# Kernel optimization log

Measured on AMD Instinct MI355X. Metric: run time of the kernel, lower is better.

The kernel has to match this reference:

```python
import jax, jax.numpy as jnp
import numpy as np

K = 2  # num_experts_per_token


def setup_inputs() -> dict:
    key = jax.random.key(0)
    ks = jax.random.split(key, 5)
    B, T, D, E, H = 2, 2048, 768, 8, 1536
    x = jax.random.normal(ks[0], (B, T, D), dtype=jnp.float32)
    gate_w = jax.random.normal(ks[1], (E, D), dtype=jnp.float32) * (1.0 / np.sqrt(D))
    gate_bank = jax.random.normal(ks[2], (E, D, H), dtype=jnp.float32) * (1.0 / np.sqrt(D))
    up_bank = jax.random.normal(ks[3], (E, D, H), dtype=jnp.float32) * (1.0 / np.sqrt(D))
    down_bank = jax.random.normal(ks[4], (E, H, D), dtype=jnp.float32) * (1.0 / np.sqrt(H))
    return {"x": x, "gate_w": gate_w, "gate_bank": gate_bank,
            "up_bank": up_bank, "down_bank": down_bank}


def reference(x, gate_w, gate_bank, up_bank, down_bank):
    # x: [B,T,D]; gate_w: [E,D]; banks: [E,D,H]/[E,D,H]/[E,H,D]
    # Eval mode: no gate noise (module only adds noise when training).
    logits = jnp.einsum('btd,ed->bte', x, gate_w)                  # [B,T,E]
    probs = jax.nn.softmax(logits, axis=-1)
    selected_probs, selected_idx = jax.lax.top_k(probs, K)          # [B,T,K]
    selected_probs = selected_probs / (
        jnp.sum(selected_probs, axis=-1, keepdims=True) + 1e-8)

    a = jnp.einsum('btd,edh->bteh', x, gate_bank)                   # [B,T,E,H]
    u = jnp.einsum('btd,edh->bteh', x, up_bank)
    h = jax.nn.silu(a) * u
    y_all = jnp.einsum('bteh,ehd->bted', h, down_bank)              # [B,T,E,D]

    # Gather the top-k experts' outputs and combine with normalized weights.
    y_sel = jnp.take_along_axis(y_all, selected_idx[..., None], axis=2)  # [B,T,K,D]
    y = jnp.sum(y_sel * selected_probs[..., None], axis=2)          # [B,T,D]
    return y
```

## Files before the change

kernel.cpp:

```cpp
#include <hip/hip_runtime.h>
#include <hip/hip_bf16.h>

#define NTOK 4096
#define DDIM 768
#define EEXP 8
#define HDIM 1536
#define MBLK 128
#define MAXMB 72
#define CAP  (MAXMB * MBLK)
#define NENT (NTOK * 2)
#define RTHREADS 1024
#define EPT (NENT / RTHREADS)
#define NTTILE 6912

typedef float f32x4 __attribute__((ext_vector_type(4)));
typedef __bf16 bf16x8 __attribute__((ext_vector_type(8)));
typedef __bf16 bf16x4 __attribute__((ext_vector_type(4)));

static const size_t XB_OFF   = 0;
static const size_t GT_OFF   = 6291456;
static const size_t UT_OFF   = GT_OFF + 18874368;
static const size_t YB_OFF   = GT_OFF;
static const size_t DT_OFF   = UT_OFF + 18874368;
static const size_t HB_OFF   = DT_OFF + 18874368;
static const size_t TKI_OFF  = HB_OFF + 28311552;
static const size_t TKW_OFF  = TKI_OFF + NENT*4;
static const size_t PT_OFF   = TKW_OFF + NENT*4;
static const size_t SL_OFF   = PT_OFF + CAP*4;
static const size_t CTRL_OFF = SL_OFF + NENT*4;
static const size_t WS_NEEDED = CTRL_OFF + 1024;

#define GLOAD16(g, l) __builtin_amdgcn_global_load_lds( \
    (const __attribute__((address_space(1))) void*)(g),  \
    (__attribute__((address_space(3))) void*)(l), 16, 0, 0)

#define MFMA_BF16 __builtin_amdgcn_mfma_f32_16x16x32_bf16


__global__ __launch_bounds__(256) void gating_kernel(
    const float* __restrict__ x, const float* __restrict__ gw,
    int* __restrict__ topk_idx, float* __restrict__ topk_w,
    __bf16* __restrict__ xb)
{
    int lane = threadIdx.x & 63;
    int t = blockIdx.x * 4 + (threadIdx.x >> 6);
    const float* xr = x + (size_t)t * DDIM;
    __bf16* xbr = xb + (size_t)t * DDIM;
    float acc[EEXP];
#pragma unroll
    for (int e = 0; e < EEXP; e++) acc[e] = 0.0f;
#pragma unroll
    for (int i = 0; i < DDIM / 64; i++) {
        int d = lane + i * 64;
        float xv = xr[d];
        xbr[d] = (__bf16)xv;
#pragma unroll
        for (int e = 0; e < EEXP; e++) acc[e] += xv * gw[e * DDIM + d];
    }
#pragma unroll
    for (int e = 0; e < EEXP; e++) {
        for (int off = 32; off; off >>= 1) acc[e] += __shfl_xor(acc[e], off);
    }
    if (lane == 0) {
        float m = acc[0];
#pragma unroll
        for (int e = 1; e < EEXP; e++) m = fmaxf(m, acc[e]);
        float p[EEXP], sum = 0.0f;
#pragma unroll
        for (int e = 0; e < EEXP; e++) { p[e] = expf(acc[e] - m); sum += p[e]; }
        int i0 = 0; float b0 = acc[0];
#pragma unroll
        for (int e = 1; e < EEXP; e++) if (acc[e] > b0) { b0 = acc[e]; i0 = e; }
        int i1 = -1; float b1 = -3.4e38f;
#pragma unroll
        for (int e = 0; e < EEXP; e++) if (e != i0 && acc[e] > b1) { b1 = acc[e]; i1 = e; }
        float pr0 = p[i0] / sum, pr1 = p[i1] / sum;
        float den = pr0 + pr1 + 1e-8f;
        topk_idx[2*t]   = i0; topk_w[2*t]   = pr0 / den;
        topk_idx[2*t+1] = i1; topk_w[2*t+1] = pr1 / den;
    }
}

__global__ __launch_bounds__(RTHREADS) void mega_kernel(
    const float* __restrict__ gb, const float* __restrict__ ub,
    const float* __restrict__ db, __bf16* __restrict__ Gt,
    __bf16* __restrict__ Ut, __bf16* __restrict__ Dt,
    const int* __restrict__ topk_idx, int* __restrict__ ctrl,
    int* __restrict__ pair_token, int* __restrict__ slot_of)
{
    __shared__ float tile[64][65];
    __shared__ int wt[EEXP][16];
    __shared__ int wpre[EEXP][16];
    __shared__ int base[EEXP];

    int tid = threadIdx.x;

    if (blockIdx.x == 0) {
        int lane = tid & 63, wv = tid >> 6;
        for (int i = tid; i < CAP; i += RTHREADS) pair_token[i] = 0;

        int e_of[EPT];
        int c[EEXP];
#pragma unroll
        for (int e = 0; e < EEXP; e++) c[e] = 0;
#pragma unroll
        for (int j = 0; j < EPT; j++) {
            int e = topk_idx[tid * EPT + j];
            e_of[j] = e;
            c[e]++;
        }
        int pre[EEXP];
#pragma unroll
        for (int e = 0; e < EEXP; e++) {
            int v = c[e];
            for (int d = 1; d < 64; d <<= 1) {
                int u = __shfl_up(v, d);
                if (lane >= d) v += u;
            }
            pre[e] = v - c[e];
            if (lane == 63) wt[e][wv] = v;
        }
        __syncthreads();
        if (tid == 0) {
            int off = 0, gmb = 0;
            for (int e = 0; e < EEXP; e++) {
                int run = 0;
                for (int w = 0; w < 16; w++) { wpre[e][w] = run; run += wt[e][w]; }
                base[e] = off;
                int nmb = (run + MBLK - 1) >> 7;
                for (int i = 0; i < nmb; i++) ctrl[32 + gmb++] = e;
                off += nmb << 7;
            }
            ctrl[24] = gmb;
        }
        __syncthreads();
        int run[EEXP];
#pragma unroll
        for (int e = 0; e < EEXP; e++) run[e] = base[e] + wpre[e][wv] + pre[e];
#pragma unroll
        for (int j = 0; j < EPT; j++) {
            int ent = tid * EPT + j;
            int e = e_of[j];
            int slot = run[e]++;
            pair_token[slot] = ent >> 1;
            slot_of[ent] = slot;
        }
        return;
    }

    int bt = blockIdx.x - 1;
    int z = bt / 288, rem = bt - z * 288;
    int bank = z >> 3, e = z & 7;
    int R, C, r0, c0;
    const float* s;
    __bf16* d;
    if (bank < 2) {
        R = DDIM; C = HDIM;
        s = (bank == 0 ? gb : ub) + (size_t)e * DDIM * HDIM;
        d = (bank == 0 ? Gt : Ut) + (size_t)e * DDIM * HDIM;
        c0 = (rem % 24) * 64; r0 = (rem / 24) * 64;
    } else {
        R = HDIM; C = DDIM;
        s = db + (size_t)e * DDIM * HDIM;
        d = Dt + (size_t)e * DDIM * HDIM;
        r0 = (rem % 24) * 64; c0 = (rem / 24) * 64;
    }
    int tx = tid & 15, ty = tid >> 4;
    {
        f32x4 v = *reinterpret_cast<const f32x4*>(&s[(size_t)(r0 + ty) * C + c0 + tx * 4]);
        tile[ty][tx*4+0] = v[0]; tile[ty][tx*4+1] = v[1];
        tile[ty][tx*4+2] = v[2]; tile[ty][tx*4+3] = v[3];
    }
    __syncthreads();
    {
        bf16x4 o;
#pragma unroll
        for (int i = 0; i < 4; i++) o[i] = (__bf16)tile[tx*4+i][ty];
        *reinterpret_cast<bf16x4*>(&d[(size_t)(c0 + ty) * R + r0 + tx*4]) = o;
    }
}

__global__ __launch_bounds__(256, 2) void gateup_kernel(
    const __bf16* __restrict__ xb, const __bf16* __restrict__ Gt,
    const __bf16* __restrict__ Ut, const int* __restrict__ ctrl,
    const int* __restrict__ pair_token, __bf16* __restrict__ hbuf)
{
    int bid = blockIdx.x;
    int swz = (bid & 7) * (MAXMB * 12 / 8) + (bid >> 3);
    int mb = swz / 12, y = swz - mb * 12;
    if (mb >= ctrl[24]) return;
    int e = ctrl[32 + mb];
    int hbase = y * 128;
    const __bf16* G = Gt + (size_t)e * HDIM * DDIM;
    const __bf16* U = Ut + (size_t)e * HDIM * DDIM;

    __shared__ __bf16 lds[3 * 8192];

    int tid = threadIdx.x;
    int lane = tid & 63, w = tid >> 6;
    int wr = w >> 1, wc = w & 1;

    int lr = tid >> 3;
    int lc = ((tid & 7) ^ (lr & 7)) << 3;
    const __bf16* gA[4];
#pragma unroll
    for (int j = 0; j < 4; j++) {
        int tok = pair_token[mb * MBLK + j * 32 + lr];
        gA[j] = xb + (size_t)tok * DDIM + lc;
    }
    const __bf16* gG = G + (size_t)(hbase + lr) * DDIM + lc;
    const __bf16* gU = U + (size_t)(hbase + lr) * DDIM + lc;
    const size_t rstep = (size_t)32 * DDIM;

    f32x4 accg[4][4], accu[4][4];
#pragma unroll
    for (int m = 0; m < 4; m++)
#pragma unroll
        for (int n = 0; n < 4; n++) { accg[m][n] = (f32x4)0.0f; accu[m][n] = (f32x4)0.0f; }

#pragma unroll
    for (int kt = 0; kt < DDIM / 64; kt++) {
        const int kk = kt * 64;
#pragma unroll
        for (int j = 0; j < 4; j++)
            GLOAD16(gA[j] + kk, &lds[j * 2048 + tid * 8]);
#pragma unroll
        for (int j = 0; j < 4; j++)
            GLOAD16(gG + kk + j * rstep, &lds[8192 + j * 2048 + tid * 8]);
#pragma unroll
        for (int j = 0; j < 4; j++)
            GLOAD16(gU + kk + j * rstep, &lds[16384 + j * 2048 + tid * 8]);
        __syncthreads();

#pragma unroll
        for (int ks = 0; ks < 2; ks++) {
            int kb = ks * 32 + (lane >> 4) * 8;
            bf16x8 af[4], bg[4], bu[4];
#pragma unroll
            for (int m = 0; m < 4; m++) {
                int row = wr * 64 + m * 16 + (lane & 15);
                af[m] = *reinterpret_cast<const bf16x8*>(
                    &lds[row * 64 + (kb ^ ((row & 7) << 3))]);
            }
#pragma unroll
            for (int n = 0; n < 4; n++) {
                int col = wc * 64 + n * 16 + (lane & 15);
                int ba = col * 64 + (kb ^ ((col & 7) << 3));
                bg[n] = *reinterpret_cast<const bf16x8*>(&lds[8192 + ba]);
                bu[n] = *reinterpret_cast<const bf16x8*>(&lds[16384 + ba]);
            }
#pragma unroll
            for (int n = 0; n < 4; n++)
#pragma unroll
                for (int m = 0; m < 4; m++) {
                    accg[m][n] = MFMA_BF16(af[m], bg[n], accg[m][n], 0, 0, 0);
                    accu[m][n] = MFMA_BF16(af[m], bu[n], accu[m][n], 0, 0, 0);
                }
        }
        __syncthreads();
    }

    size_t slotbase = (size_t)mb * MBLK;
#pragma unroll
    for (int m = 0; m < 4; m++)
#pragma unroll
        for (int n = 0; n < 4; n++)
#pragma unroll
            for (int r = 0; r < 4; r++) {
                int row = wr * 64 + m * 16 + (lane >> 4) * 4 + r;
                int col = hbase + wc * 64 + n * 16 + (lane & 15);
                float a = accg[m][n][r], u = accu[m][n][r];
                float hv = (a / (1.0f + expf(-a))) * u;
                hbuf[(slotbase + row) * HDIM + col] = (__bf16)hv;
            }
}

__global__ __launch_bounds__(256, 3) void down_kernel(
    const __bf16* __restrict__ hbuf, const __bf16* __restrict__ Dt,
    const int* __restrict__ ctrl, float* __restrict__ ybuf)
{
    int bid = blockIdx.x;
    int swz = (bid & 7) * (MAXMB * 6 / 8) + (bid >> 3);
    int mb = swz / 6, y = swz - mb * 6;
    if (mb >= ctrl[24]) return;
    int e = ctrl[32 + mb];
    int dbase = y * 128;
    const __bf16* Dn = Dt + (size_t)e * DDIM * HDIM;

    __shared__ __bf16 lds[2 * 8192];

    int tid = threadIdx.x;
    int lane = tid & 63, w = tid >> 6;
    int wr = w >> 1, wc = w & 1;

    int lr = tid >> 3;
    int lc = ((tid & 7) ^ (lr & 7)) << 3;
    const __bf16* gA = hbuf + (size_t)(mb * MBLK + lr) * HDIM + lc;
    const __bf16* gB = Dn + (size_t)(dbase + lr) * HDIM + lc;
    const size_t rstep = (size_t)32 * HDIM;

    f32x4 acc[4][4];
#pragma unroll
    for (int m = 0; m < 4; m++)
#pragma unroll
        for (int n = 0; n < 4; n++) acc[m][n] = (f32x4)0.0f;

#pragma unroll
    for (int kt = 0; kt < HDIM / 64; kt++) {
        const int kk = kt * 64;
#pragma unroll
        for (int j = 0; j < 4; j++)
            GLOAD16(gA + kk + j * rstep, &lds[j * 2048 + tid * 8]);
#pragma unroll
        for (int j = 0; j < 4; j++)
            GLOAD16(gB + kk + j * rstep, &lds[8192 + j * 2048 + tid * 8]);
        __syncthreads();

#pragma unroll
        for (int ks = 0; ks < 2; ks++) {
            int kb = ks * 32 + (lane >> 4) * 8;
            bf16x8 af[4], bd[4];
#pragma unroll
            for (int m = 0; m < 4; m++) {
                int row = wr * 64 + m * 16 + (lane & 15);
                af[m] = *reinterpret_cast<const bf16x8*>(
                    &lds[row * 64 + (kb ^ ((row & 7) << 3))]);
            }
#pragma unroll
            for (int n = 0; n < 4; n++) {
                int col = wc * 64 + n * 16 + (lane & 15);
                bd[n] = *reinterpret_cast<const bf16x8*>(
                    &lds[8192 + col * 64 + (kb ^ ((col & 7) << 3))]);
            }
#pragma unroll
            for (int n = 0; n < 4; n++)
#pragma unroll
                for (int m = 0; m < 4; m++)
                    acc[m][n] = MFMA_BF16(af[m], bd[n], acc[m][n], 0, 0, 0);
        }
        __syncthreads();
    }

#pragma unroll
    for (int m = 0; m < 4; m++)
#pragma unroll
        for (int n = 0; n < 4; n++)
#pragma unroll
            for (int r = 0; r < 4; r++) {
                int row = wr * 64 + m * 16 + (lane >> 4) * 4 + r;
                int col = dbase + wc * 64 + n * 16 + (lane & 15);
                ybuf[(size_t)(mb * MBLK + row) * DDIM + col] = acc[m][n][r];
            }
}

__global__ __launch_bounds__(192) void combine_kernel(
    const float* __restrict__ ybuf, const int* __restrict__ slot_of,
    const float* __restrict__ topk_w, float* __restrict__ out)
{
    int t = blockIdx.x;
    int q = threadIdx.x;
    int s0 = slot_of[2*t], s1 = slot_of[2*t+1];
    float w0 = topk_w[2*t], w1 = topk_w[2*t+1];
    f32x4 y0 = reinterpret_cast<const f32x4*>(ybuf + (size_t)s0 * DDIM)[q];
    f32x4 y1 = reinterpret_cast<const f32x4*>(ybuf + (size_t)s1 * DDIM)[q];
    f32x4 o;
#pragma unroll
    for (int r = 0; r < 4; r++) o[r] = w0 * y0[r] + w1 * y1[r];
    reinterpret_cast<f32x4*>(out + (size_t)t * DDIM)[q] = o;
}

extern "C" void kernel_launch(void* const* d_in, const int* in_sizes, int n_in,
                              void* d_out, int out_size, void* d_ws, size_t ws_size,
                              hipStream_t stream)
{
    if (ws_size < WS_NEEDED) return;

    const float* x      = (const float*)d_in[0];
    const float* gate_w = (const float*)d_in[1];
    const float* gbank  = (const float*)d_in[2];
    const float* ubank  = (const float*)d_in[3];
    const float* dbank  = (const float*)d_in[4];
    float* out = (float*)d_out;

    char* ws = (char*)d_ws;
    __bf16* xb   = (__bf16*)(ws + XB_OFF);
    __bf16* Gt   = (__bf16*)(ws + GT_OFF);
    __bf16* Ut   = (__bf16*)(ws + UT_OFF);
    float*  ybuf = (float*)(ws + YB_OFF);
    __bf16* Dt   = (__bf16*)(ws + DT_OFF);
    __bf16* hbuf = (__bf16*)(ws + HB_OFF);
    int*    tki  = (int*)(ws + TKI_OFF);
    float*  tkw  = (float*)(ws + TKW_OFF);
    int*    pt   = (int*)(ws + PT_OFF);
    int*    slot = (int*)(ws + SL_OFF);
    int*    ctrl = (int*)(ws + CTRL_OFF);

    gating_kernel<<<NTOK / 4, 256, 0, stream>>>(x, gate_w, tki, tkw, xb);
    mega_kernel<<<NTTILE + 1, RTHREADS, 0, stream>>>(
        gbank, ubank, dbank, Gt, Ut, Dt, tki, ctrl, pt, slot);

    gateup_kernel<<<MAXMB * (HDIM / 128), 256, 0, stream>>>(xb, Gt, Ut, ctrl, pt, hbuf);
    down_kernel<<<MAXMB * (DDIM / 128), 256, 0, stream>>>(hbuf, Dt, ctrl, ybuf);
    combine_kernel<<<NTOK, 192, 0, stream>>>(ybuf, slot, tkw, out);
}
```

Baseline: 125.4 us.

## Switch GEMMs to 32x32x16 MFMA and fuse gating into weight-transpose prep kernel

Both grouped GEMM kernels now use the 32x32x16 bf16 MFMA with 2x2 fragments per wave instead of 4x4 fragments of 16x16x32, which halves the LDS fragment reads per k-step. The gating/top-k work is merged into the transpose kernel as extra blocks, and routing is split into a separate single-block kernel. The transpose blocks drop from 1024 to 256 threads, each handling four rows. Together this cuts LDS traffic and gives better occupancy in the prep phase, at the cost of one extra launch for routing.

```diff
diff --git a/kernel.cpp b/kernel.cpp
--- a/kernel.cpp
+++ b/kernel.cpp
@@ -11,9 +11,11 @@
 #define NENT (NTOK * 2)
 #define RTHREADS 1024
 #define EPT (NENT / RTHREADS)
+#define NGATE (NTOK / 4)
 #define NTTILE 6912
 
 typedef float f32x4 __attribute__((ext_vector_type(4)));
+typedef float f32x16 __attribute__((ext_vector_type(16)));
 typedef __bf16 bf16x8 __attribute__((ext_vector_type(8)));
 typedef __bf16 bf16x4 __attribute__((ext_vector_type(4)));
 
@@ -34,121 +36,62 @@
     (const __attribute__((address_space(1))) void*)(g),  \
     (__attribute__((address_space(3))) void*)(l), 16, 0, 0)
 
-#define MFMA_BF16 __builtin_amdgcn_mfma_f32_16x16x32_bf16
-
-
-__global__ __launch_bounds__(256) void gating_kernel(
+#define MFMA32 __builtin_amdgcn_mfma_f32_32x32x16_bf16
+
+
+__global__ __launch_bounds__(256) void prep_kernel(
     const float* __restrict__ x, const float* __restrict__ gw,
     int* __restrict__ topk_idx, float* __restrict__ topk_w,
-    __bf16* __restrict__ xb)
-{
-    int lane = threadIdx.x & 63;
-    int t = blockIdx.x * 4 + (threadIdx.x >> 6);
-    const float* xr = x + (size_t)t * DDIM;
-    __bf16* xbr = xb + (size_t)t * DDIM;
-    float acc[EEXP];
-#pragma unroll
-    for (int e = 0; e < EEXP; e++) acc[e] = 0.0f;
-#pragma unroll
-    for (int i = 0; i < DDIM / 64; i++) {
-        int d = lane + i * 64;
-        float xv = xr[d];
-        xbr[d] = (__bf16)xv;
-#pragma unroll
-        for (int e = 0; e < EEXP; e++) acc[e] += xv * gw[e * DDIM + d];
-    }
-#pragma unroll
-    for (int e = 0; e < EEXP; e++) {
-        for (int off = 32; off; off >>= 1) acc[e] += __shfl_xor(acc[e], off);
-    }
-    if (lane == 0) {
-        float m = acc[0];
-#pragma unroll
-        for (int e = 1; e < EEXP; e++) m = fmaxf(m, acc[e]);
-        float p[EEXP], sum = 0.0f;
-#pragma unroll
-        for (int e = 0; e < EEXP; e++) { p[e] = expf(acc[e] - m); sum += p[e]; }
-        int i0 = 0; float b0 = acc[0];
-#pragma unroll
-        for (int e = 1; e < EEXP; e++) if (acc[e] > b0) { b0 = acc[e]; i0 = e; }
-        int i1 = -1; float b1 = -3.4e38f;
-#pragma unroll
-        for (int e = 0; e < EEXP; e++) if (e != i0 && acc[e] > b1) { b1 = acc[e]; i1 = e; }
-        float pr0 = p[i0] / sum, pr1 = p[i1] / sum;
-        float den = pr0 + pr1 + 1e-8f;
-        topk_idx[2*t]   = i0; topk_w[2*t]   = pr0 / den;
-        topk_idx[2*t+1] = i1; topk_w[2*t+1] = pr1 / den;
-    }
-}
-
-__global__ __launch_bounds__(RTHREADS) void mega_kernel(
+    __bf16* __restrict__ xb,
     const float* __restrict__ gb, const float* __restrict__ ub,
     const float* __restrict__ db, __bf16* __restrict__ Gt,
-    __bf16* __restrict__ Ut, __bf16* __restrict__ Dt,
-    const int* __restrict__ topk_idx, int* __restrict__ ctrl,
-    int* __restrict__ pair_token, int* __restrict__ slot_of)
+    __bf16* __restrict__ Ut, __bf16* __restrict__ Dt)
 {
     __shared__ float tile[64][65];
-    __shared__ int wt[EEXP][16];
-    __shared__ int wpre[EEXP][16];
-    __shared__ int base[EEXP];
-
     int tid = threadIdx.x;
 
-    if (blockIdx.x == 0) {
-        int lane = tid & 63, wv = tid >> 6;
-        for (int i = tid; i < CAP; i += RTHREADS) pair_token[i] = 0;
-
-        int e_of[EPT];
-        int c[EEXP];
-#pragma unroll
-        for (int e = 0; e < EEXP; e++) c[e] = 0;
-#pragma unroll
-        for (int j = 0; j < EPT; j++) {
-            int e = topk_idx[tid * EPT + j];
-            e_of[j] = e;
-            c[e]++;
-        }
-        int pre[EEXP];
+    if (blockIdx.x < NGATE) {
+        int lane = tid & 63;
+        int t = blockIdx.x * 4 + (tid >> 6);
+        const float* xr = x + (size_t)t * DDIM;
+        __bf16* xbr = xb + (size_t)t * DDIM;
+        float acc[EEXP];
+#pragma unroll
+        for (int e = 0; e < EEXP; e++) acc[e] = 0.0f;
+#pragma unroll
+        for (int i = 0; i < DDIM / 64; i++) {
+            int d = lane + i * 64;
+            float xv = xr[d];
+            xbr[d] = (__bf16)xv;
+#pragma unroll
+            for (int e = 0; e < EEXP; e++) acc[e] += xv * gw[e * DDIM + d];
+        }
 #pragma unroll
         for (int e = 0; e < EEXP; e++) {
-            int v = c[e];
-            for (int d = 1; d < 64; d <<= 1) {
-                int u = __shfl_up(v, d);
-                if (lane >= d) v += u;
-            }
-            pre[e] = v - c[e];
-            if (lane == 63) wt[e][wv] = v;
-        }
-        __syncthreads();
-        if (tid == 0) {
-            int off = 0, gmb = 0;
-            for (int e = 0; e < EEXP; e++) {
-                int run = 0;
-                for (int w = 0; w < 16; w++) { wpre[e][w] = run; run += wt[e][w]; }
-                base[e] = off;
-                int nmb = (run + MBLK - 1) >> 7;
-                for (int i = 0; i < nmb; i++) ctrl[32 + gmb++] = e;
-                off += nmb << 7;
-            }
-            ctrl[24] = gmb;
-        }
-        __syncthreads();
-        int run[EEXP];
-#pragma unroll
-        for (int e = 0; e < EEXP; e++) run[e] = base[e] + wpre[e][wv] + pre[e];
-#pragma unroll
-        for (int j = 0; j < EPT; j++) {
-            int ent = tid * EPT + j;
-            int e = e_of[j];
-            int slot = run[e]++;
-            pair_token[slot] = ent >> 1;
-            slot_of[ent] = slot;
+            for (int off = 32; off; off >>= 1) acc[e] += __shfl_xor(acc[e], off);
+        }
+        if (lane == 0) {
+            float m = acc[0];
+#pragma unroll
+            for (int e = 1; e < EEXP; e++) m = fmaxf(m, acc[e]);
+            float p[EEXP], sum = 0.0f;
+#pragma unroll
+            for (int e = 0; e < EEXP; e++) { p[e] = expf(acc[e] - m); sum += p[e]; }
+            int i0 = 0; float b0 = acc[0];
+#pragma unroll
+            for (int e = 1; e < EEXP; e++) if (acc[e] > b0) { b0 = acc[e]; i0 = e; }
+            int i1 = -1; float b1 = -3.4e38f;
+#pragma unroll
+            for (int e = 0; e < EEXP; e++) if (e != i0 && acc[e] > b1) { b1 = acc[e]; i1 = e; }
+            float pr0 = p[i0] / sum, pr1 = p[i1] / sum;
+            float den = pr0 + pr1 + 1e-8f;
+            topk_idx[2*t]   = i0; topk_w[2*t]   = pr0 / den;
+            topk_idx[2*t+1] = i1; topk_w[2*t+1] = pr1 / den;
         }
         return;
     }
 
-    int bt = blockIdx.x - 1;
+    int bt = blockIdx.x - NGATE;
     int z = bt / 288, rem = bt - z * 288;
     int bank = z >> 3, e = z & 7;
     int R, C, r0, c0;
@@ -166,17 +109,82 @@
         r0 = (rem % 24) * 64; c0 = (rem / 24) * 64;
     }
     int tx = tid & 15, ty = tid >> 4;
-    {
-        f32x4 v = *reinterpret_cast<const f32x4*>(&s[(size_t)(r0 + ty) * C + c0 + tx * 4]);
-        tile[ty][tx*4+0] = v[0]; tile[ty][tx*4+1] = v[1];
-        tile[ty][tx*4+2] = v[2]; tile[ty][tx*4+3] = v[3];
+#pragma unroll
+    for (int j = 0; j < 4; j++) {
+        int r = ty + j * 16;
+        f32x4 v = *reinterpret_cast<const f32x4*>(&s[(size_t)(r0 + r) * C + c0 + tx * 4]);
+        tile[r][tx*4+0] = v[0]; tile[r][tx*4+1] = v[1];
+        tile[r][tx*4+2] = v[2]; tile[r][tx*4+3] = v[3];
     }
     __syncthreads();
-    {
+#pragma unroll
+    for (int j = 0; j < 4; j++) {
+        int c = ty + j * 16;
         bf16x4 o;
 #pragma unroll
-        for (int i = 0; i < 4; i++) o[i] = (__bf16)tile[tx*4+i][ty];
-        *reinterpret_cast<bf16x4*>(&d[(size_t)(c0 + ty) * R + r0 + tx*4]) = o;
+        for (int i = 0; i < 4; i++) o[i] = (__bf16)tile[tx*4+i][c];
+        *reinterpret_cast<bf16x4*>(&d[(size_t)(c0 + c) * R + r0 + tx*4]) = o;
+    }
+}
+
+__global__ __launch_bounds__(RTHREADS) void route_kernel(
+    const int* __restrict__ topk_idx, int* __restrict__ ctrl,
+    int* __restrict__ pair_token, int* __restrict__ slot_of)
+{
+    __shared__ int wt[EEXP][16];
+    __shared__ int wpre[EEXP][16];
+    __shared__ int base[EEXP];
+
+    int tid = threadIdx.x;
+    int lane = tid & 63, wv = tid >> 6;
+
+    for (int i = tid; i < CAP; i += RTHREADS) pair_token[i] = 0;
+
+    int e_of[EPT];
+    int c[EEXP];
+#pragma unroll
+    for (int e = 0; e < EEXP; e++) c[e] = 0;
+#pragma unroll
+    for (int j = 0; j < EPT; j++) {
+        int e = topk_idx[tid * EPT + j];
+        e_of[j] = e;
+        c[e]++;
+    }
+    int pre[EEXP];
+#pragma unroll
+    for (int e = 0; e < EEXP; e++) {
+        int v = c[e];
+        for (int d = 1; d < 64; d <<= 1) {
+            int u = __shfl_up(v, d);
+            if (lane >= d) v += u;
+        }
+        pre[e] = v - c[e];
+        if (lane == 63) wt[e][wv] = v;
+    }
+    __syncthreads();
+    if (tid == 0) {
+        int off = 0, gmb = 0;
+        for (int e = 0; e < EEXP; e++) {
+            int run = 0;
+            for (int w = 0; w < 16; w++) { wpre[e][w] = run; run += wt[e][w]; }
+            base[e] = off;
+            int nmb = (run + MBLK - 1) >> 7;
+            for (int i = 0; i < nmb; i++) ctrl[32 + gmb++] = e;
+            off += nmb << 7;
+        }
+        ctrl[24] = gmb;
+    }
+    __syncthreads();
+    int run[EEXP];
+#pragma unroll
+    for (int e = 0; e < EEXP; e++) run[e] = base[e] + wpre[e][wv] + pre[e];
+#pragma unroll
+    for (int j = 0; j < EPT; j++) {
+        int ent = tid * EPT + j;
+        int e = e_of[j];
+        int slot = run[e]++;
+        pair_token[slot] = ent >> 1;
+        slot_of[ent] = slot;
     }
 }
 
@@ -212,11 +220,11 @@
     const __bf16* gU = U + (size_t)(hbase + lr) * DDIM + lc;
     const size_t rstep = (size_t)32 * DDIM;
 
-    f32x4 accg[4][4], accu[4][4];
-#pragma unroll
-    for (int m = 0; m < 4; m++)
-#pragma unroll
-        for (int n = 0; n < 4; n++) { accg[m][n] = (f32x4)0.0f; accu[m][n] = (f32x4)0.0f; }
+    f32x16 accg[2][2], accu[2][2];
+#pragma unroll
+    for (int m = 0; m < 2; m++)
+#pragma unroll
+        for (int n = 0; n < 2; n++) { accg[m][n] = (f32x16)0.0f; accu[m][n] = (f32x16)0.0f; }
 
 #pragma unroll
     for (int kt = 0; kt < DDIM / 64; kt++) {
@@ -233,42 +241,43 @@
         __syncthreads();
 
 #pragma unroll
-        for (int ks = 0; ks < 2; ks++) {
-            int kb = ks * 32 + (lane >> 4) * 8;
-            bf16x8 af[4], bg[4], bu[4];
-#pragma unroll
-            for (int m = 0; m < 4; m++) {
-                int row = wr * 64 + m * 16 + (lane & 15);
+        for (int s = 0; s < 4; s++) {
+            int kb = s * 16 + (lane >> 5) * 8;
+            bf16x8 af[2], bg[2], bu[2];
+#pragma unroll
+            for (int m = 0; m < 2; m++) {
+                int row = wr * 64 + m * 32 + (lane & 31);
                 af[m] = *reinterpret_cast<const bf16x8*>(
                     &lds[row * 64 + (kb ^ ((row & 7) << 3))]);
             }
 #pragma unroll
-            for (int n = 0; n < 4; n++) {
-                int col = wc * 64 + n * 16 + (lane & 15);
+            for (int n = 0; n < 2; n++) {
+                int col = wc * 64 + n * 32 + (lane & 31);
                 int ba = col * 64 + (kb ^ ((col & 7) << 3));
                 bg[n] = *reinterpret_cast<const bf16x8*>(&lds[8192 + ba]);
                 bu[n] = *reinterpret_cast<const bf16x8*>(&lds[16384 + ba]);
             }
 #pragma unroll
-            for (int n = 0; n < 4; n++)
-#pragma unroll
-                for (int m = 0; m < 4; m++) {
-                    accg[m][n] = MFMA_BF16(af[m], bg[n], accg[m][n], 0, 0, 0);
-                    accu[m][n] = MFMA_BF16(af[m], bu[n], accu[m][n], 0, 0, 0);
+            for (int n = 0; n < 2; n++)
+#pragma unroll
+                for (int m = 0; m < 2; m++) {
+                    accg[m][n] = MFMA32(af[m], bg[n], accg[m][n], 0, 0, 0);
+                    accu[m][n] = MFMA32(af[m], bu[n], accu[m][n], 0, 0, 0);
                 }
         }
         __syncthreads();
     }
 
     size_t slotbase = (size_t)mb * MBLK;
-#pragma unroll
-    for (int m = 0; m < 4; m++)
-#pragma unroll
-        for (int n = 0; n < 4; n++)
-#pragma unroll
-            for (int r = 0; r < 4; r++) {
-                int row = wr * 64 + m * 16 + (lane >> 4) * 4 + r;
-                int col = hbase + wc * 64 + n * 16 + (lane & 15);
+    int hi4 = (lane >> 5) * 4;
+#pragma unroll
+    for (int m = 0; m < 2; m++)
+#pragma unroll
+        for (int n = 0; n < 2; n++)
+#pragma unroll
+            for (int r = 0; r < 16; r++) {
+                int row = wr * 64 + m * 32 + (r & 3) + 8 * (r >> 2) + hi4;
+                int col = hbase + wc * 64 + n * 32 + (lane & 31);
                 float a = accg[m][n][r], u = accu[m][n][r];
                 float hv = (a / (1.0f + expf(-a))) * u;
                 hbuf[(slotbase + row) * HDIM + col] = (__bf16)hv;
@@ -299,11 +308,11 @@
     const __bf16* gB = Dn + (size_t)(dbase + lr) * HDIM + lc;
     const size_t rstep = (size_t)32 * HDIM;
 
-    f32x4 acc[4][4];
-#pragma unroll
-    for (int m = 0; m < 4; m++)
-#pragma unroll
-        for (int n = 0; n < 4; n++) acc[m][n] = (f32x4)0.0f;
+    f32x16 acc[2][2];
+#pragma unroll
+    for (int m = 0; m < 2; m++)
+#pragma unroll
+        for (int n = 0; n < 2; n++) acc[m][n] = (f32x16)0.0f;
 
 #pragma unroll
     for (int kt = 0; kt < HDIM / 64; kt++) {
@@ -317,38 +326,39 @@
         __syncthreads();
 
 #pragma unroll
-        for (int ks = 0; ks < 2; ks++) {
-            int kb = ks * 32 + (lane >> 4) * 8;
-            bf16x8 af[4], bd[4];
-#pragma unroll
-            for (int m = 0; m < 4; m++) {
-                int row = wr * 64 + m * 16 + (lane & 15);
+        for (int s = 0; s < 4; s++) {
+            int kb = s * 16 + (lane >> 5) * 8;
+            bf16x8 af[2], bd[2];
+#pragma unroll
+            for (int m = 0; m < 2; m++) {
+                int row = wr * 64 + m * 32 + (lane & 31);
                 af[m] = *reinterpret_cast<const bf16x8*>(
                     &lds[row * 64 + (kb ^ ((row & 7) << 3))]);
             }
 #pragma unroll
-            for (int n = 0; n < 4; n++) {
-                int col = wc * 64 + n * 16 + (lane & 15);
+            for (int n = 0; n < 2; n++) {
+                int col = wc * 64 + n * 32 + (lane & 31);
                 bd[n] = *reinterpret_cast<const bf16x8*>(
                     &lds[8192 + col * 64 + (kb ^ ((col & 7) << 3))]);
             }
 #pragma unroll
-            for (int n = 0; n < 4; n++)
-#pragma unroll
-                for (int m = 0; m < 4; m++)
-                    acc[m][n] = MFMA_BF16(af[m], bd[n], acc[m][n], 0, 0, 0);
+            for (int n = 0; n < 2; n++)
+#pragma unroll
+                for (int m = 0; m < 2; m++)
+                    acc[m][n] = MFMA32(af[m], bd[n], acc[m][n], 0, 0, 0);
         }
         __syncthreads();
     }
 
-#pragma unroll
-    for (int m = 0; m < 4; m++)
-#pragma unroll
-        for (int n = 0; n < 4; n++)
-#pragma unroll
-            for (int r = 0; r < 4; r++) {
-                int row = wr * 64 + m * 16 + (lane >> 4) * 4 + r;
-                int col = dbase + wc * 64 + n * 16 + (lane & 15);
+    int hi4 = (lane >> 5) * 4;
+#pragma unroll
+    for (int m = 0; m < 2; m++)
+#pragma unroll
+        for (int n = 0; n < 2; n++)
+#pragma unroll
+            for (int r = 0; r < 16; r++) {
+                int row = wr * 64 + m * 32 + (r & 3) + 8 * (r >> 2) + hi4;
+                int col = dbase + wc * 64 + n * 32 + (lane & 31);
                 ybuf[(size_t)(mb * MBLK + row) * DDIM + col] = acc[m][n][r];
             }
 }
@@ -395,9 +405,9 @@
     int*    slot = (int*)(ws + SL_OFF);
     int*    ctrl = (int*)(ws + CTRL_OFF);
 
-    gating_kernel<<<NTOK / 4, 256, 0, stream>>>(x, gate_w, tki, tkw, xb);
-    mega_kernel<<<NTTILE + 1, RTHREADS, 0, stream>>>(
-        gbank, ubank, dbank, Gt, Ut, Dt, tki, ctrl, pt, slot);
+    prep_kernel<<<NGATE + NTTILE, 256, 0, stream>>>(
+        x, gate_w, tki, tkw, xb, gbank, ubank, dbank, Gt, Ut, Dt);
+    route_kernel<<<1, RTHREADS, 0, stream>>>(tki, ctrl, pt, slot);
 
     gateup_kernel<<<MAXMB * (HDIM / 128), 256, 0, stream>>>(xb, Gt, Ut, ctrl, pt, hbuf);
     down_kernel<<<MAXMB * (DDIM / 128), 256, 0, stream>>>(hbuf, Dt, ctrl, ybuf);
```

New measurement: 141.0 us. 12.5% more time.

## Fuse gating into transpose kernel, split routing out, store expert outputs as bf16

Applied to the files above, without the earlier changes.

Gating and the weight transpose/convert now run as one kernel launch with 256-thread blocks, each handling a 64x64 tile with four rows per thread. The routing scan moves into its own single-block kernel that runs after gating completes. The down-projection now writes its per-slot outputs in bf16 instead of fp32, which halves ybuf traffic in down_kernel and combine_kernel. In exchange the stream gains an extra launch and a single-block serial step, and the expert outputs lose precision before the weighted combine.

```diff
diff --git a/kernel.cpp b/kernel.cpp
--- a/kernel.cpp
+++ b/kernel.cpp
@@ -11,6 +11,7 @@
 #define NENT (NTOK * 2)
 #define RTHREADS 1024
 #define EPT (NENT / RTHREADS)
+#define NGATE (NTOK / 4)
 #define NTTILE 6912
 
 typedef float f32x4 __attribute__((ext_vector_type(4)));
@@ -37,118 +38,59 @@
 #define MFMA_BF16 __builtin_amdgcn_mfma_f32_16x16x32_bf16
 
 
-__global__ __launch_bounds__(256) void gating_kernel(
+__global__ __launch_bounds__(256) void prep_kernel(
     const float* __restrict__ x, const float* __restrict__ gw,
     int* __restrict__ topk_idx, float* __restrict__ topk_w,
-    __bf16* __restrict__ xb)
-{
-    int lane = threadIdx.x & 63;
-    int t = blockIdx.x * 4 + (threadIdx.x >> 6);
-    const float* xr = x + (size_t)t * DDIM;
-    __bf16* xbr = xb + (size_t)t * DDIM;
-    float acc[EEXP];
-#pragma unroll
-    for (int e = 0; e < EEXP; e++) acc[e] = 0.0f;
-#pragma unroll
-    for (int i = 0; i < DDIM / 64; i++) {
-        int d = lane + i * 64;
-        float xv = xr[d];
-        xbr[d] = (__bf16)xv;
-#pragma unroll
-        for (int e = 0; e < EEXP; e++) acc[e] += xv * gw[e * DDIM + d];
-    }
-#pragma unroll
-    for (int e = 0; e < EEXP; e++) {
-        for (int off = 32; off; off >>= 1) acc[e] += __shfl_xor(acc[e], off);
-    }
-    if (lane == 0) {
-        float m = acc[0];
-#pragma unroll
-        for (int e = 1; e < EEXP; e++) m = fmaxf(m, acc[e]);
-        float p[EEXP], sum = 0.0f;
-#pragma unroll
-        for (int e = 0; e < EEXP; e++) { p[e] = expf(acc[e] - m); sum += p[e]; }
-        int i0 = 0; float b0 = acc[0];
-#pragma unroll
-        for (int e = 1; e < EEXP; e++) if (acc[e] > b0) { b0 = acc[e]; i0 = e; }
-        int i1 = -1; float b1 = -3.4e38f;
-#pragma unroll
-        for (int e = 0; e < EEXP; e++) if (e != i0 && acc[e] > b1) { b1 = acc[e]; i1 = e; }
-        float pr0 = p[i0] / sum, pr1 = p[i1] / sum;
-        float den = pr0 + pr1 + 1e-8f;
-        topk_idx[2*t]   = i0; topk_w[2*t]   = pr0 / den;
-        topk_idx[2*t+1] = i1; topk_w[2*t+1] = pr1 / den;
-    }
-}
-
-__global__ __launch_bounds__(RTHREADS) void mega_kernel(
+    __bf16* __restrict__ xb,
     const float* __restrict__ gb, const float* __restrict__ ub,
     const float* __restrict__ db, __bf16* __restrict__ Gt,
-    __bf16* __restrict__ Ut, __bf16* __restrict__ Dt,
-    const int* __restrict__ topk_idx, int* __restrict__ ctrl,
-    int* __restrict__ pair_token, int* __restrict__ slot_of)
+    __bf16* __restrict__ Ut, __bf16* __restrict__ Dt)
 {
     __shared__ float tile[64][65];
-    __shared__ int wt[EEXP][16];
-    __shared__ int wpre[EEXP][16];
-    __shared__ int base[EEXP];
-
     int tid = threadIdx.x;
 
-    if (blockIdx.x == 0) {
-        int lane = tid & 63, wv = tid >> 6;
-        for (int i = tid; i < CAP; i += RTHREADS) pair_token[i] = 0;
-
-        int e_of[EPT];
-        int c[EEXP];
-#pragma unroll
-        for (int e = 0; e < EEXP; e++) c[e] = 0;
-#pragma unroll
-        for (int j = 0; j < EPT; j++) {
-            int e = topk_idx[tid * EPT + j];
-            e_of[j] = e;
-            c[e]++;
-        }
-        int pre[EEXP];
+    if (blockIdx.x < NGATE) {
+        int lane = tid & 63;
+        int t = blockIdx.x * 4 + (tid >> 6);
+        const float* xr = x + (size_t)t * DDIM;
+        __bf16* xbr = xb + (size_t)t * DDIM;
+        float acc[EEXP];
+#pragma unroll
+        for (int e = 0; e < EEXP; e++) acc[e] = 0.0f;
+#pragma unroll
+        for (int i = 0; i < DDIM / 64; i++) {
+            int d = lane + i * 64;
+            float xv = xr[d];
+            xbr[d] = (__bf16)xv;
+#pragma unroll
+            for (int e = 0; e < EEXP; e++) acc[e] += xv * gw[e * DDIM + d];
+        }
 #pragma unroll
         for (int e = 0; e < EEXP; e++) {
-            int v = c[e];
-            for (int d = 1; d < 64; d <<= 1) {
-                int u = __shfl_up(v, d);
-                if (lane >= d) v += u;
-            }
-            pre[e] = v - c[e];
-            if (lane == 63) wt[e][wv] = v;
-        }
-        __syncthreads();
-        if (tid == 0) {
-            int off = 0, gmb = 0;
-            for (int e = 0; e < EEXP; e++) {
-                int run = 0;
-                for (int w = 0; w < 16; w++) { wpre[e][w] = run; run += wt[e][w]; }
-                base[e] = off;
-                int nmb = (run + MBLK - 1) >> 7;
-                for (int i = 0; i < nmb; i++) ctrl[32 + gmb++] = e;
-                off += nmb << 7;
-            }
-            ctrl[24] = gmb;
-        }
-        __syncthreads();
-        int run[EEXP];
-#pragma unroll
-        for (int e = 0; e < EEXP; e++) run[e] = base[e] + wpre[e][wv] + pre[e];
-#pragma unroll
-        for (int j = 0; j < EPT; j++) {
-            int ent = tid * EPT + j;
-            int e = e_of[j];
-            int slot = run[e]++;
-            pair_token[slot] = ent >> 1;
-            slot_of[ent] = slot;
+            for (int off = 32; off; off >>= 1) acc[e] += __shfl_xor(acc[e], off);
+        }
+        if (lane == 0) {
+            float m = acc[0];
+#pragma unroll
+            for (int e = 1; e < EEXP; e++) m = fmaxf(m, acc[e]);
+            float p[EEXP], sum = 0.0f;
+#pragma unroll
+            for (int e = 0; e < EEXP; e++) { p[e] = expf(acc[e] - m); sum += p[e]; }
+            int i0 = 0; float b0 = acc[0];
+#pragma unroll
+            for (int e = 1; e < EEXP; e++) if (acc[e] > b0) { b0 = acc[e]; i0 = e; }
+            int i1 = -1; float b1 = -3.4e38f;
+#pragma unroll
+            for (int e = 0; e < EEXP; e++) if (e != i0 && acc[e] > b1) { b1 = acc[e]; i1 = e; }
+            float pr0 = p[i0] / sum, pr1 = p[i1] / sum;
+            float den = pr0 + pr1 + 1e-8f;
+            topk_idx[2*t]   = i0; topk_w[2*t]   = pr0 / den;
+            topk_idx[2*t+1] = i1; topk_w[2*t+1] = pr1 / den;
         }
         return;
     }
 
-    int bt = blockIdx.x - 1;
+    int bt = blockIdx.x - NGATE;
     int z = bt / 288, rem = bt - z * 288;
     int bank = z >> 3, e = z & 7;
     int R, C, r0, c0;
@@ -166,17 +108,82 @@
         r0 = (rem % 24) * 64; c0 = (rem / 24) * 64;
     }
     int tx = tid & 15, ty = tid >> 4;
-    {
-        f32x4 v = *reinterpret_cast<const f32x4*>(&s[(size_t)(r0 + ty) * C + c0 + tx * 4]);
-        tile[ty][tx*4+0] = v[0]; tile[ty][tx*4+1] = v[1];
-        tile[ty][tx*4+2] = v[2]; tile[ty][tx*4+3] = v[3];
+#pragma unroll
+    for (int j = 0; j < 4; j++) {
+        int r = ty + j * 16;
+        f32x4 v = *reinterpret_cast<const f32x4*>(&s[(size_t)(r0 + r) * C + c0 + tx * 4]);
+        tile[r][tx*4+0] = v[0]; tile[r][tx*4+1] = v[1];
+        tile[r][tx*4+2] = v[2]; tile[r][tx*4+3] = v[3];
     }
     __syncthreads();
-    {
+#pragma unroll
+    for (int j = 0; j < 4; j++) {
+        int c = ty + j * 16;
         bf16x4 o;
 #pragma unroll
-        for (int i = 0; i < 4; i++) o[i] = (__bf16)tile[tx*4+i][ty];
-        *reinterpret_cast<bf16x4*>(&d[(size_t)(c0 + ty) * R + r0 + tx*4]) = o;
+        for (int i = 0; i < 4; i++) o[i] = (__bf16)tile[tx*4+i][c];
+        *reinterpret_cast<bf16x4*>(&d[(size_t)(c0 + c) * R + r0 + tx*4]) = o;
+    }
+}
+
+__global__ __launch_bounds__(RTHREADS) void route_kernel(
+    const int* __restrict__ topk_idx, int* __restrict__ ctrl,
+    int* __restrict__ pair_token, int* __restrict__ slot_of)
+{
+    __shared__ int wt[EEXP][16];
+    __shared__ int wpre[EEXP][16];
+    __shared__ int base[EEXP];
+
+    int tid = threadIdx.x;
+    int lane = tid & 63, wv = tid >> 6;
+
+    for (int i = tid; i < CAP; i += RTHREADS) pair_token[i] = 0;
+
+    int e_of[EPT];
+    int c[EEXP];
+#pragma unroll
+    for (int e = 0; e < EEXP; e++) c[e] = 0;
+#pragma unroll
+    for (int j = 0; j < EPT; j++) {
+        int e = topk_idx[tid * EPT + j];
+        e_of[j] = e;
+        c[e]++;
+    }
+    int pre[EEXP];
+#pragma unroll
+    for (int e = 0; e < EEXP; e++) {
+        int v = c[e];
+        for (int d = 1; d < 64; d <<= 1) {
+            int u = __shfl_up(v, d);
+            if (lane >= d) v += u;
+        }
+        pre[e] = v - c[e];
+        if (lane == 63) wt[e][wv] = v;
+    }
+    __syncthreads();
+    if (tid == 0) {
+        int off = 0, gmb = 0;
+        for (int e = 0; e < EEXP; e++) {
+            int run = 0;
+            for (int w = 0; w < 16; w++) { wpre[e][w] = run; run += wt[e][w]; }
+            base[e] = off;
+            int nmb = (run + MBLK - 1) >> 7;
+            for (int i = 0; i < nmb; i++) ctrl[32 + gmb++] = e;
+            off += nmb << 7;
+        }
+        ctrl[24] = gmb;
+    }
+    __syncthreads();
+    int run[EEXP];
+#pragma unroll
+    for (int e = 0; e < EEXP; e++) run[e] = base[e] + wpre[e][wv] + pre[e];
+#pragma unroll
+    for (int j = 0; j < EPT; j++) {
+        int ent = tid * EPT + j;
+        int e = e_of[j];
+        int slot = run[e]++;
+        pair_token[slot] = ent >> 1;
+        slot_of[ent] = slot;
     }
 }
 
@@ -277,7 +284,7 @@
 
 __global__ __launch_bounds__(256, 3) void down_kernel(
     const __bf16* __restrict__ hbuf, const __bf16* __restrict__ Dt,
-    const int* __restrict__ ctrl, float* __restrict__ ybuf)
+    const int* __restrict__ ctrl, __bf16* __restrict__ ybuf)
 {
     int bid = blockIdx.x;
     int swz = (bid & 7) * (MAXMB * 6 / 8) + (bid >> 3);
@@ -349,23 +356,23 @@
             for (int r = 0; r < 4; r++) {
                 int row = wr * 64 + m * 16 + (lane >> 4) * 4 + r;
                 int col = dbase + wc * 64 + n * 16 + (lane & 15);
-                ybuf[(size_t)(mb * MBLK + row) * DDIM + col] = acc[m][n][r];
+                ybuf[(size_t)(mb * MBLK + row) * DDIM + col] = (__bf16)acc[m][n][r];
             }
 }
 
 __global__ __launch_bounds__(192) void combine_kernel(
-    const float* __restrict__ ybuf, const int* __restrict__ slot_of,
+    const __bf16* __restrict__ ybuf, const int* __restrict__ slot_of,
     const float* __restrict__ topk_w, float* __restrict__ out)
 {
     int t = blockIdx.x;
     int q = threadIdx.x;
     int s0 = slot_of[2*t], s1 = slot_of[2*t+1];
     float w0 = topk_w[2*t], w1 = topk_w[2*t+1];
-    f32x4 y0 = reinterpret_cast<const f32x4*>(ybuf + (size_t)s0 * DDIM)[q];
-    f32x4 y1 = reinterpret_cast<const f32x4*>(ybuf + (size_t)s1 * DDIM)[q];
+    bf16x4 y0 = reinterpret_cast<const bf16x4*>(ybuf + (size_t)s0 * DDIM)[q];
+    bf16x4 y1 = reinterpret_cast<const bf16x4*>(ybuf + (size_t)s1 * DDIM)[q];
     f32x4 o;
 #pragma unroll
-    for (int r = 0; r < 4; r++) o[r] = w0 * y0[r] + w1 * y1[r];
+    for (int r = 0; r < 4; r++) o[r] = w0 * (float)y0[r] + w1 * (float)y1[r];
     reinterpret_cast<f32x4*>(out + (size_t)t * DDIM)[q] = o;
 }
 
@@ -386,7 +393,7 @@
     __bf16* xb   = (__bf16*)(ws + XB_OFF);
     __bf16* Gt   = (__bf16*)(ws + GT_OFF);
     __bf16* Ut   = (__bf16*)(ws + UT_OFF);
-    float*  ybuf = (float*)(ws + YB_OFF);
+    __bf16* ybuf = (__bf16*)(ws + YB_OFF);
     __bf16* Dt   = (__bf16*)(ws + DT_OFF);
     __bf16* hbuf = (__bf16*)(ws + HB_OFF);
     int*    tki  = (int*)(ws + TKI_OFF);
@@ -395,9 +402,9 @@
     int*    slot = (int*)(ws + SL_OFF);
     int*    ctrl = (int*)(ws + CTRL_OFF);
 
-    gating_kernel<<<NTOK / 4, 256, 0, stream>>>(x, gate_w, tki, tkw, xb);
-    mega_kernel<<<NTTILE + 1, RTHREADS, 0, stream>>>(
-        gbank, ubank, dbank, Gt, Ut, Dt, tki, ctrl, pt, slot);
+    prep_kernel<<<NGATE + NTTILE, 256, 0, stream>>>(
+        x, gate_w, tki, tkw, xb, gbank, ubank, dbank, Gt, Ut, Dt);
+    route_kernel<<<1, RTHREADS, 0, stream>>>(tki, ctrl, pt, slot);
 
     gateup_kernel<<<MAXMB * (HDIM / 128), 256, 0, stream>>>(xb, Gt, Ut, ctrl, pt, hbuf);
     down_kernel<<<MAXMB * (DDIM / 128), 256, 0, stream>>>(hbuf, Dt, ctrl, ybuf);
```

Measured after the change: 127.6 us (median of 3 runs). About the same (+1.8%).
